# Optimization experiments

Measured on AMD Instinct MI355X. Metric: run time of the kernel, lower is better.

Reference implementation:

```python
import jax, jax.numpy as jnp
import numpy as np

B, S, H = 32, 2048, 1024


def setup_inputs() -> dict:
    key = jax.random.key(0)
    k1, k2, k3, k4, k5, k6 = jax.random.split(key, 6)
    hidden = jax.random.normal(k1, (B, H), dtype=jnp.float32)
    encoder_outputs = jax.random.normal(k2, (B, S, H), dtype=jnp.float32)
    lengths = jax.random.randint(k3, (B,), 1, S + 1, dtype=jnp.int64)
    scale = 1.0 / np.sqrt(H)
    Wq = jax.random.normal(k4, (H, H), dtype=jnp.float32) * scale
    Wk = jax.random.normal(k5, (H, H), dtype=jnp.float32) * scale
    v = jax.random.uniform(k6, (H,), dtype=jnp.float32)  # torch.rand init
    return {"hidden": hidden, "encoder_outputs": encoder_outputs,
            "lengths": lengths, "Wq": Wq, "Wk": Wk, "v": v}


def reference(hidden, encoder_outputs, lengths, Wq, Wk, v):
    # query: (B, 1, H); nn.Linear(bias=False) applies x @ W.T
    query = (hidden @ Wq.T)[:, None, :]
    keys = jnp.einsum('bsh,kh->bsk', encoder_outputs, Wk)  # (B, S, H)
    energy = jnp.tanh(query + keys)                         # (B, S, H)
    attn = jnp.einsum('bsh,h->bs', energy, v)               # (B, S)
    seq = encoder_outputs.shape[1]
    mask = jnp.arange(seq)[None, :] < lengths[:, None]      # (B, S)
    attn = jnp.where(mask, attn, -jnp.inf)
    return jax.nn.softmax(attn, axis=1)
```

## Files before the change

### kernel.cpp

```cpp
#include <hip/hip_runtime.h>
#include <hip/hip_fp16.h>
#include <stdint.h>

#define B_SZ 32
#define S_SZ 2048
#define H_SZ 1024
#define M_SZ (B_SZ * S_SZ)

typedef _Float16 half8 __attribute__((ext_vector_type(8)));
typedef float floatx4 __attribute__((ext_vector_type(4)));

struct h4 { _Float16 x, y, z, w; };

__global__ __launch_bounds__(256) void convert_f32_to_f16(
    const float* __restrict__ in, h4* __restrict__ out, int n4) {
  int i = blockIdx.x * blockDim.x + threadIdx.x;
  int stride = gridDim.x * blockDim.x;
  const float4* in4 = (const float4*)in;
  for (; i < n4; i += stride) {
    float4 f = in4[i];
    h4 o;
    o.x = (_Float16)f.x; o.y = (_Float16)f.y;
    o.z = (_Float16)f.z; o.w = (_Float16)f.w;
    out[i] = o;
  }
}

__global__ __launch_bounds__(256) void query_kernel(
    const float* __restrict__ hidden, const float* __restrict__ Wq,
    float* __restrict__ q) {
  int t = blockIdx.x * blockDim.x + threadIdx.x;
  int b = t & 31;
  int n = t >> 5;
  const float4* h4p = (const float4*)(hidden + (size_t)b * H_SZ);
  const float4* w4p = (const float4*)(Wq + (size_t)n * H_SZ);
  float acc = 0.f;
  #pragma unroll 4
  for (int i = 0; i < H_SZ / 4; ++i) {
    float4 h = h4p[i], w = w4p[i];
    acc = fmaf(h.x, w.x, acc);
    acc = fmaf(h.y, w.y, acc);
    acc = fmaf(h.z, w.z, acc);
    acc = fmaf(h.w, w.w, acc);
  }
  q[(size_t)b * H_SZ + n] = acc;
}

__device__ __forceinline__ void gl_lds16(const void* g, void* l) {
  __builtin_amdgcn_global_load_lds(
      (const __attribute__((address_space(1))) void*)g,
      (__attribute__((address_space(3))) void*)l,
      16, 0, 0);
}

__device__ __forceinline__ float fast_tanh(float x) {
  float ax = fabsf(x);
  float e = __expf(ax * -2.0f);
  float t = (1.0f - e) / (1.0f + e);
  return copysignf(t, x);
}

#define TILE 128
#define BK 32
#define NT (H_SZ / BK)

__global__ __launch_bounds__(256, 3) void fused_keys_kernel(
    const float* __restrict__ A,
    const _Float16* __restrict__ Bt,
    const float* __restrict__ q,
    const float* __restrict__ v,
    float* __restrict__ partial)
{
  __shared__ __align__(16) _Float16 As[2][TILE * BK];
  __shared__ __align__(16) _Float16 Bs[3][TILE * BK];
  __shared__ float q_l[TILE];
  __shared__ float v_l[TILE];

  const int tid  = threadIdx.x;
  const int w    = tid >> 6;
  const int lane = tid & 63;

  const int hw   = blockIdx.x;
  const int xcd  = hw & 7;
  const int slot = hw >> 3;
  const int bn   = slot & 7;
  const int bm   = ((slot >> 3) << 3) | xcd;

  const int R0   = bm * TILE;
  const int C0   = bn * TILE;
  const int bidx = R0 >> 11;

  if (tid < TILE) {
    q_l[tid] = q[(size_t)bidx * H_SZ + C0 + tid];
    v_l[tid] = v[C0 + tid];
  }

  const int cL   = lane & 15, quad = lane >> 4;
  const int sB   = (cL >> 1) & 3;

  floatx4 acc[2][8];
  #pragma unroll
  for (int m = 0; m < 2; ++m)
    #pragma unroll
    for (int n = 0; n < 8; ++n)
      acc[m][n] = (floatx4){0.f, 0.f, 0.f, 0.f};

  const int arow = w * 32 + (lane >> 1);
  const int ah   = lane & 1;
  const int akey = (lane >> 2) & 3;
  const int ap0  = (2 * ah)     ^ akey;
  const int ap1  = (2 * ah + 1) ^ akey;
  const float* Asrc = A + (size_t)(R0 + arow) * H_SZ + ah * 16;

  const int brow_l = lane >> 2;
  const int bp     = lane & 3;
  const _Float16* Bblk = Bt + (size_t)C0 * H_SZ;

  float4 ar[2][4];

  auto stageB = [&](int kt2, int b) {
    const int kof = kt2 * BK;
    #pragma unroll
    for (int j = 0; j < 2; ++j) {
      const int row = w * 32 + j * 16 + brow_l;
      const int cg  = bp ^ ((row >> 1) & 3);
      gl_lds16(Bblk + (size_t)row * H_SZ + kof + cg * 8,
               (char*)&Bs[b][0] + (w * 128 + j * 64) * 16);
    }
  };

  auto loadA = [&](int kt2, int s) {
    const float4* p = (const float4*)(Asrc + kt2 * BK);
    ar[s][0] = p[0]; ar[s][1] = p[1]; ar[s][2] = p[2]; ar[s][3] = p[3];
  };

  auto writeA = [&](int s, int b) {
    half8 h0 = (half8){(_Float16)ar[s][0].x, (_Float16)ar[s][0].y, (_Float16)ar[s][0].z, (_Float16)ar[s][0].w,
                       (_Float16)ar[s][1].x, (_Float16)ar[s][1].y, (_Float16)ar[s][1].z, (_Float16)ar[s][1].w};
    half8 h1 = (half8){(_Float16)ar[s][2].x, (_Float16)ar[s][2].y, (_Float16)ar[s][2].z, (_Float16)ar[s][2].w,
                       (_Float16)ar[s][3].x, (_Float16)ar[s][3].y, (_Float16)ar[s][3].z, (_Float16)ar[s][3].w};
    _Float16* dst = &As[b][arow * BK];
    *(half8*)(dst + ap0 * 8) = h0;
    *(half8*)(dst + ap1 * 8) = h1;
  };

  auto compute = [&](int ab, int bb) {
    half8 af[2], bf[8];
    #pragma unroll
    for (int m = 0; m < 2; ++m) {
      const int r = w * 32 + m * 16 + cL;
      af[m] = *(const half8*)(&As[ab][r * BK] + ((quad ^ sB) << 3));
    }
    #pragma unroll
    for (int n = 0; n < 8; ++n) {
      const int r = n * 16 + cL;
      bf[n] = *(const half8*)(&Bs[bb][r * BK] + ((quad ^ sB) << 3));
    }
    __builtin_amdgcn_s_setprio(1);
    #pragma unroll
    for (int m = 0; m < 2; ++m)
      #pragma unroll
      for (int n = 0; n < 8; ++n)
        acc[m][n] = __builtin_amdgcn_mfma_f32_16x16x32_f16(af[m], bf[n], acc[m][n], 0, 0, 0);
    __builtin_amdgcn_s_setprio(0);
  };

  stageB(0, 0);
  asm volatile("" ::: "memory");
  loadA(0, 0);
  stageB(1, 1);
  asm volatile("" ::: "memory");
  loadA(1, 1);
  writeA(0, 0);
  asm volatile("s_waitcnt lgkmcnt(0)" ::: "memory");
  __builtin_amdgcn_s_barrier();

  #pragma unroll
  for (int t = 0; t < NT; ++t) {
    if (t + 2 < NT) {
      stageB(t + 2, (t + 2) % 3);
      asm volatile("" ::: "memory");
      loadA(t + 2, t & 1);
    }
    compute(t & 1, t % 3);
    if (t + 1 < NT) {
      writeA((t + 1) & 1, (t + 1) & 1);
      asm volatile("s_waitcnt lgkmcnt(0)" ::: "memory");
      __builtin_amdgcn_s_barrier();
    }
  }

  float qv[8], vv[8];
  #pragma unroll
  for (int n = 0; n < 8; ++n) {
    const int col = n * 16 + cL;
    qv[n] = q_l[col];
    vv[n] = v_l[col];
  }
  #pragma unroll
  for (int m = 0; m < 2; ++m) {
    #pragma unroll
    for (int r = 0; r < 4; ++r) {
      float s = 0.f;
      #pragma unroll
      for (int n = 0; n < 8; ++n)
        s += vv[n] * fast_tanh(qv[n] + acc[m][n][r]);
      s += __shfl_xor(s, 1);
      s += __shfl_xor(s, 2);
      s += __shfl_xor(s, 4);
      s += __shfl_xor(s, 8);
      if (cL == 0)
        partial[(size_t)bn * M_SZ + R0 + w * 32 + m * 16 + quad * 4 + r] = s;
    }
  }
}

__global__ __launch_bounds__(256) void softmax_kernel(
    const float* __restrict__ partial, const int* __restrict__ lengths,
    float* __restrict__ out) {
  __shared__ float wred[4];
  __shared__ float wsum[4];
  const int b = blockIdx.x;
  const int tid = threadIdx.x;
  const int len = lengths[b];

  float lg[8];
  #pragma unroll
  for (int i = 0; i < 8; ++i) {
    const int s = tid + i * 256;
    const size_t row = (size_t)b * S_SZ + s;
    float l = 0.f;
    #pragma unroll
    for (int nt = 0; nt < 8; ++nt) l += partial[(size_t)nt * M_SZ + row];
    lg[i] = (s < len) ? l : -INFINITY;
  }

  float mx = lg[0];
  #pragma unroll
  for (int i = 1; i < 8; ++i) mx = fmaxf(mx, lg[i]);
  #pragma unroll
  for (int off = 32; off; off >>= 1) mx = fmaxf(mx, __shfl_xor(mx, off));
  if ((tid & 63) == 0) wred[tid >> 6] = mx;
  __syncthreads();
  mx = fmaxf(fmaxf(wred[0], wred[1]), fmaxf(wred[2], wred[3]));

  float pe[8];
  float sum = 0.f;
  #pragma unroll
  for (int i = 0; i < 8; ++i) {
    float e = (lg[i] == -INFINITY) ? 0.f : __expf(lg[i] - mx);
    pe[i] = e;
    sum += e;
  }
  #pragma unroll
  for (int off = 32; off; off >>= 1) sum += __shfl_xor(sum, off);
  if ((tid & 63) == 0) wsum[tid >> 6] = sum;
  __syncthreads();
  sum = wsum[0] + wsum[1] + wsum[2] + wsum[3];
  const float inv = 1.0f / sum;

  #pragma unroll
  for (int i = 0; i < 8; ++i) {
    const int s = tid + i * 256;
    out[(size_t)b * S_SZ + s] = pe[i] * inv;
  }
}

extern "C" void kernel_launch(void* const* d_in, const int* in_sizes, int n_in,
                              void* d_out, int out_size, void* d_ws, size_t ws_size,
                              hipStream_t stream) {
  const float* hidden  = (const float*)d_in[0];
  const float* enc     = (const float*)d_in[1];
  const int*   lengths = (const int*)d_in[2];
  const float* Wq      = (const float*)d_in[3];
  const float* Wk      = (const float*)d_in[4];
  const float* v       = (const float*)d_in[5];
  float* out = (float*)d_out;

  char* ws = (char*)d_ws;
  _Float16* B16     = (_Float16*)ws;
  float*    q       = (float*)(ws + 2097152);
  float*    partial = (float*)(ws + 2097152 + 131072);

  convert_f32_to_f16<<<1024, 256, 0, stream>>>(Wk, (h4*)B16, (H_SZ * H_SZ) / 4);
  query_kernel<<<128, 256, 0, stream>>>(hidden, Wq, q);
  fused_keys_kernel<<<(M_SZ / TILE) * (H_SZ / TILE), 256, 0, stream>>>(enc, B16, q, v, partial);
  softmax_kernel<<<B_SZ, 256, 0, stream>>>(partial, lengths, out);
}
```

Before: 648.3 us.

## Load A fragments directly from global into registers, dropping the A LDS stage

```diff
diff --git a/kernel.cpp b/kernel.cpp
--- a/kernel.cpp
+++ b/kernel.cpp
@@ -64,14 +64,13 @@
 #define BK 32
 #define NT (H_SZ / BK)
 
-__global__ __launch_bounds__(256, 3) void fused_keys_kernel(
+__global__ __launch_bounds__(256, 4) void fused_keys_kernel(
     const float* __restrict__ A,
     const _Float16* __restrict__ Bt,
     const float* __restrict__ q,
     const float* __restrict__ v,
     float* __restrict__ partial)
 {
-  __shared__ __align__(16) _Float16 As[2][TILE * BK];
   __shared__ __align__(16) _Float16 Bs[3][TILE * BK];
   __shared__ float q_l[TILE];
   __shared__ float v_l[TILE];
@@ -105,18 +104,21 @@
     for (int n = 0; n < 8; ++n)
       acc[m][n] = (floatx4){0.f, 0.f, 0.f, 0.f};
 
-  const int arow = w * 32 + (lane >> 1);
-  const int ah   = lane & 1;
-  const int akey = (lane >> 2) & 3;
-  const int ap0  = (2 * ah)     ^ akey;
-  const int ap1  = (2 * ah + 1) ^ akey;
-  const float* Asrc = A + (size_t)(R0 + arow) * H_SZ + ah * 16;
+  const float* Af0 = A + (size_t)(R0 + w * 32 +  0 + cL) * H_SZ + 8 * quad;
+  const float* Af1 = A + (size_t)(R0 + w * 32 + 16 + cL) * H_SZ + 8 * quad;
+
+  float4 arf[4];
+
+  auto loadAfrag = [&](int kt2) {
+    const float4* p0 = (const float4*)(Af0 + kt2 * BK);
+    const float4* p1 = (const float4*)(Af1 + kt2 * BK);
+    arf[0] = p0[0]; arf[1] = p0[1];
+    arf[2] = p1[0]; arf[3] = p1[1];
+  };
 
   const int brow_l = lane >> 2;
   const int bp     = lane & 3;
   const _Float16* Bblk = Bt + (size_t)C0 * H_SZ;
-
-  float4 ar[2][4];
 
   auto stageB = [&](int kt2, int b) {
     const int kof = kt2 * BK;
@@ -129,62 +131,43 @@
     }
   };
 
-  auto loadA = [&](int kt2, int s) {
-    const float4* p = (const float4*)(Asrc + kt2 * BK);
-    ar[s][0] = p[0]; ar[s][1] = p[1]; ar[s][2] = p[2]; ar[s][3] = p[3];
-  };
-
-  auto writeA = [&](int s, int b) {
-    half8 h0 = (half8){(_Float16)ar[s][0].x, (_Float16)ar[s][0].y, (_Float16)ar[s][0].z, (_Float16)ar[s][0].w,
-                       (_Float16)ar[s][1].x, (_Float16)ar[s][1].y, (_Float16)ar[s][1].z, (_Float16)ar[s][1].w};
-    half8 h1 = (half8){(_Float16)ar[s][2].x, (_Float16)ar[s][2].y, (_Float16)ar[s][2].z, (_Float16)ar[s][2].w,
-                       (_Float16)ar[s][3].x, (_Float16)ar[s][3].y, (_Float16)ar[s][3].z, (_Float16)ar[s][3].w};
-    _Float16* dst = &As[b][arow * BK];
-    *(half8*)(dst + ap0 * 8) = h0;
-    *(half8*)(dst + ap1 * 8) = h1;
-  };
-
-  auto compute = [&](int ab, int bb) {
-    half8 af[2], bf[8];
-    #pragma unroll
-    for (int m = 0; m < 2; ++m) {
-      const int r = w * 32 + m * 16 + cL;
-      af[m] = *(const half8*)(&As[ab][r * BK] + ((quad ^ sB) << 3));
-    }
-    #pragma unroll
-    for (int n = 0; n < 8; ++n) {
-      const int r = n * 16 + cL;
-      bf[n] = *(const half8*)(&Bs[bb][r * BK] + ((quad ^ sB) << 3));
-    }
-    __builtin_amdgcn_s_setprio(1);
-    #pragma unroll
-    for (int m = 0; m < 2; ++m)
+  stageB(0, 0);
+  stageB(1, 1);
+  loadAfrag(0);
+  __syncthreads();
+
+  #pragma unroll
+  for (int t = 0; t < NT; ++t) {
+    if (t + 2 < NT)
+      stageB(t + 2, (t + 2) % 3);
+
+    half8 af0 = (half8){(_Float16)arf[0].x, (_Float16)arf[0].y, (_Float16)arf[0].z, (_Float16)arf[0].w,
+                        (_Float16)arf[1].x, (_Float16)arf[1].y, (_Float16)arf[1].z, (_Float16)arf[1].w};
+    half8 af1 = (half8){(_Float16)arf[2].x, (_Float16)arf[2].y, (_Float16)arf[2].z, (_Float16)arf[2].w,
+                        (_Float16)arf[3].x, (_Float16)arf[3].y, (_Float16)arf[3].z, (_Float16)arf[3].w};
+
+    if (t + 1 < NT)
+      loadAfrag(t + 1);
+
+    const int bb = t % 3;
+    #pragma unroll
+    for (int g = 0; g < 2; ++g) {
+      half8 bf[4];
       #pragma unroll
-      for (int n = 0; n < 8; ++n)
-        acc[m][n] = __builtin_amdgcn_mfma_f32_16x16x32_f16(af[m], bf[n], acc[m][n], 0, 0, 0);
-    __builtin_amdgcn_s_setprio(0);
-  };
-
-  stageB(0, 0);
-  asm volatile("" ::: "memory");
-  loadA(0, 0);
-  stageB(1, 1);
-  asm volatile("" ::: "memory");
-  loadA(1, 1);
-  writeA(0, 0);
-  asm volatile("s_waitcnt lgkmcnt(0)" ::: "memory");
-  __builtin_amdgcn_s_barrier();
-
-  #pragma unroll
-  for (int t = 0; t < NT; ++t) {
-    if (t + 2 < NT) {
-      stageB(t + 2, (t + 2) % 3);
-      asm volatile("" ::: "memory");
-      loadA(t + 2, t & 1);
-    }
-    compute(t & 1, t % 3);
+      for (int n = 0; n < 4; ++n) {
+        const int r = (g * 4 + n) * 16 + cL;
+        bf[n] = *(const half8*)(&Bs[bb][r * BK] + ((quad ^ sB) << 3));
+      }
+      __builtin_amdgcn_s_setprio(1);
+      #pragma unroll
+      for (int n = 0; n < 4; ++n) {
+        acc[0][g * 4 + n] = __builtin_amdgcn_mfma_f32_16x16x32_f16(af0, bf[n], acc[0][g * 4 + n], 0, 0, 0);
+        acc[1][g * 4 + n] = __builtin_amdgcn_mfma_f32_16x16x32_f16(af1, bf[n], acc[1][g * 4 + n], 0, 0, 0);
+      }
+      __builtin_amdgcn_s_setprio(0);
+    }
+
     if (t + 1 < NT) {
-      writeA((t + 1) & 1, (t + 1) & 1);
       asm volatile("s_waitcnt lgkmcnt(0)" ::: "memory");
       __builtin_amdgcn_s_barrier();
     }
```

Result: no change. 650.5 us (+0.3%).
